# Kernel tuning notes

Hardware: AMD Instinct MI355X
Metric: run time of the kernel (lower is better)

The kernel has to match this reference:

```python
import jax, jax.numpy as jnp
import numpy as np

GRID_SHAPE = (32, 32)
TEMPERATURE = 1.0


def setup_inputs() -> dict:
    key = jax.random.key(0)
    k1, k2 = jax.random.split(key)
    x = jax.random.normal(k1, (16384, 1024), dtype=jnp.float32)
    som_weights = jax.random.normal(k2, (*GRID_SHAPE, 1024), dtype=jnp.float32) * 0.05
    return {"x": x, "som_weights": som_weights}


def reference(x, som_weights):
    # x: [B, D]; som_weights: [G1, G2, D]
    B, D = x.shape
    g1, g2 = GRID_SHAPE
    w_flat = som_weights.reshape(g1 * g2, D)  # [N, D]
    x_sq = jnp.sum(x * x, axis=-1, keepdims=True)          # [B, 1]
    w_sq = jnp.sum(w_flat * w_flat, axis=-1)[None, :]       # [1, N]
    d2 = x_sq - 2.0 * (x @ w_flat.T) + w_sq                 # [B, N]
    logits = (-d2 / TEMPERATURE).reshape(B, g1, g2)         # [B, G1, G2]
    # per-dimension softmax along each spatial axis, combined multiplicatively
    s1 = jax.nn.softmax(logits, axis=1)
    s2 = jax.nn.softmax(logits, axis=2)
    combined = s1 * s2
    combined = combined / (jnp.sum(combined, axis=(1, 2), keepdims=True) + 1e-8)
    # soft reconstruction: weighted sum over grid of codebook vectors
    recon = jnp.einsum('bn,nd->bd', combined.reshape(B, g1 * g2), w_flat)
    return recon
```

## Files before the change

kernel.cpp:

```cpp
#include <hip/hip_runtime.h>
#include <hip/hip_bf16.h>

static constexpr int BATCH = 16384;
static constexpr int DIM   = 1024;
static constexpr int NN    = 1024;
static constexpr int G     = 32;

typedef _Float16 half8  __attribute__((ext_vector_type(8)));
typedef _Float16 half4v __attribute__((ext_vector_type(4)));
typedef float    f32x4  __attribute__((ext_vector_type(4)));

__global__ __launch_bounds__(256) void transpose_w_kernel(const float* __restrict__ W,
                                                          _Float16* __restrict__ Wh,
                                                          _Float16* __restrict__ WTh) {
    __shared__ _Float16 tile[64][72];
    const int t  = threadIdx.x;
    const int n0 = (blockIdx.x & 15) * 64;
    const int d0 = (blockIdx.x >> 4) * 64;
#pragma unroll
    for (int p = 0; p < 4; ++p) {
        int n = n0 + p * 16 + (t >> 4);
        int d = d0 + (t & 15) * 4;
        float4 v = *(const float4*)(W + (size_t)n * DIM + d);
        half4v h;
        h[0] = (_Float16)v.x; h[1] = (_Float16)v.y;
        h[2] = (_Float16)v.z; h[3] = (_Float16)v.w;
        *(half4v*)(Wh + (size_t)n * DIM + d) = h;
#pragma unroll
        for (int k = 0; k < 4; ++k)
            tile[(t & 15) * 4 + k][p * 16 + (t >> 4)] = h[k];
    }
    __syncthreads();
#pragma unroll
    for (int p = 0; p < 4; ++p) {
        int dp = p * 16 + (t >> 4);
        int nc = (t & 15) * 4;
        half4v hv = *(const half4v*)&tile[dp][nc];
        *(half4v*)(WTh + (size_t)(d0 + dp) * NN + n0 + nc) = hv;
    }
}

__global__ __launch_bounds__(256) void wsq_kernel(const float* __restrict__ W,
                                                  float* __restrict__ wsq) {
    const int n = blockIdx.x;
    const int t = threadIdx.x;
    float4 v = *(const float4*)(W + (size_t)n * DIM + 4 * t);
    float ss = v.x * v.x + v.y * v.y + v.z * v.z + v.w * v.w;
#pragma unroll
    for (int o = 32; o > 0; o >>= 1) ss += __shfl_xor(ss, o, 64);
    __shared__ float red[4];
    if ((t & 63) == 0) red[t >> 6] = ss;
    __syncthreads();
    if (t == 0) wsq[n] = red[0] + red[1] + red[2] + red[3];
}

template <typename AT, int EPI>
__global__ __launch_bounds__(256) void gemm_bt_kernel(const AT* __restrict__ A,
                                                      const _Float16* __restrict__ B,
                                                      float* __restrict__ C,
                                                      const float* __restrict__ wsq,
                                                      int M, int N, int K) {
    constexpr bool AF32 = sizeof(AT) == 4;
    __shared__ __align__(16) AT       As[128 * 64];
    __shared__ __align__(16) _Float16 Bs[128 * 64];

    const int t  = threadIdx.x;
    const int l  = t & 63;
    const int wv = t >> 6;

    const int NT  = N >> 7;
    const int MT  = M >> 7;
    const int lid = blockIdx.x;
    const int xcd = lid & 7;
    const int i0  = lid >> 3;
    const int bn  = (i0 % NT) * 128;
    const int bm  = (xcd * (MT >> 3) + i0 / NT) * 128;

    const int wm = (wv >> 1) * 64;
    const int wn = (wv & 1) * 64;

    auto stage = [&](int k0) {
        if constexpr (AF32) {
#pragma unroll
            for (int j = 0; j < 8; ++j) {
                int rbase = wv * 32 + j * 4;
                int row   = rbase + (l >> 4);
                int c     = (l & 15) ^ (row & 15);
                const float* gA = (const float*)A + (size_t)(bm + row) * K + k0 + c * 4;
                __builtin_amdgcn_global_load_lds(
                    (const __attribute__((address_space(1))) void*)gA,
                    (__attribute__((address_space(3))) void*)((float*)As + rbase * 64),
                    16, 0, 0);
            }
        } else {
#pragma unroll
            for (int j = 0; j < 4; ++j) {
                int rbase = wv * 32 + j * 8;
                int row   = rbase + (l >> 3);
                int c     = (l & 7) ^ (row & 7);
                const _Float16* gA = (const _Float16*)A + (size_t)(bm + row) * K + k0 + c * 8;
                __builtin_amdgcn_global_load_lds(
                    (const __attribute__((address_space(1))) void*)gA,
                    (__attribute__((address_space(3))) void*)((_Float16*)As + rbase * 64),
                    16, 0, 0);
            }
        }
#pragma unroll
        for (int j = 0; j < 4; ++j) {
            int rbase = wv * 32 + j * 8;
            int row   = rbase + (l >> 3);
            int c     = (l & 7) ^ (row & 7);
            const _Float16* gB = B + (size_t)(bn + row) * K + k0 + c * 8;
            __builtin_amdgcn_global_load_lds(
                (const __attribute__((address_space(1))) void*)gB,
                (__attribute__((address_space(3))) void*)(Bs + rbase * 64),
                16, 0, 0);
        }
    };

    f32x4 acc[4][4] = {};
    stage(0);

    for (int kt = 0; kt < K; kt += 64) {
        __syncthreads();
#pragma unroll
        for (int sub = 0; sub < 2; ++sub) {
            half8 af[4], bf[4];
#pragma unroll
            for (int mi = 0; mi < 4; ++mi) {
                if constexpr (AF32) {
                    const float* pa = (const float*)As + (wm + (l & 15) + mi * 16) * 64;
                    int cpair = sub * 8 + (l >> 4) * 2;
                    f32x4 lo = *(const f32x4*)(pa + ((cpair     ) ^ (l & 15)) * 4);
                    f32x4 hi = *(const f32x4*)(pa + ((cpair + 1) ^ (l & 15)) * 4);
#pragma unroll
                    for (int q = 0; q < 4; ++q) {
                        af[mi][q]     = (_Float16)lo[q];
                        af[mi][4 + q] = (_Float16)hi[q];
                    }
                } else {
                    const _Float16* pa = (const _Float16*)As + (wm + (l & 15) + mi * 16) * 64;
                    int c = sub * 4 + (l >> 4);
                    af[mi] = *(const half8*)(pa + (c ^ (l & 7)) * 8);
                }
            }
#pragma unroll
            for (int ni = 0; ni < 4; ++ni) {
                const _Float16* pb = Bs + (wn + (l & 15) + ni * 16) * 64;
                int c = sub * 4 + (l >> 4);
                bf[ni] = *(const half8*)(pb + (c ^ (l & 7)) * 8);
            }
#pragma unroll
            for (int mi = 0; mi < 4; ++mi)
#pragma unroll
                for (int ni = 0; ni < 4; ++ni)
                    acc[mi][ni] = __builtin_amdgcn_mfma_f32_16x16x32_f16(
                        af[mi], bf[ni], acc[mi][ni], 0, 0, 0);
        }
        __syncthreads();
        if (kt + 64 < K) stage(kt + 64);
    }

#pragma unroll
    for (int mi = 0; mi < 4; ++mi) {
        const int rbase = bm + wm + mi * 16 + (l >> 4) * 4;
#pragma unroll
        for (int ni = 0; ni < 4; ++ni) {
            const int col = bn + wn + ni * 16 + (l & 15);
            float wq = (EPI == 1) ? wsq[col] : 0.f;
#pragma unroll
            for (int r = 0; r < 4; ++r) {
                float v = acc[mi][ni][r];
                if (EPI == 1) v = 2.f * v - wq;
                C[(size_t)(rbase + r) * N + col] = v;
            }
        }
    }
}

__global__ __launch_bounds__(256) void softmax_kernel(const float* __restrict__ L,
                                                      _Float16* __restrict__ Ch) {
    const int l  = threadIdx.x & 63;
    const int wv = threadIdx.x >> 6;
    const int b  = blockIdx.x * 4 + wv;

    const f32x4* Lr = (const f32x4*)(L + (size_t)b * NN);
    f32x4 v[4];
#pragma unroll
    for (int i = 0; i < 4; ++i) v[i] = Lr[i * 64 + l];

    float er[4][4], ec[4][4];
    float rinv[4];
#pragma unroll
    for (int i = 0; i < 4; ++i) {
        float m = fmaxf(fmaxf(v[i][0], v[i][1]), fmaxf(v[i][2], v[i][3]));
        m = fmaxf(m, __shfl_xor(m, 1, 64));
        m = fmaxf(m, __shfl_xor(m, 2, 64));
        m = fmaxf(m, __shfl_xor(m, 4, 64));
        float s = 0.f;
#pragma unroll
        for (int j = 0; j < 4; ++j) { er[i][j] = __expf(v[i][j] - m); s += er[i][j]; }
        s += __shfl_xor(s, 1, 64);
        s += __shfl_xor(s, 2, 64);
        s += __shfl_xor(s, 4, 64);
        rinv[i] = 1.f / s;
    }
#pragma unroll
    for (int j = 0; j < 4; ++j) {
        float m = fmaxf(fmaxf(v[0][j], v[1][j]), fmaxf(v[2][j], v[3][j]));
        m = fmaxf(m, __shfl_xor(m, 8, 64));
        m = fmaxf(m, __shfl_xor(m, 16, 64));
        m = fmaxf(m, __shfl_xor(m, 32, 64));
        float s = 0.f;
#pragma unroll
        for (int i = 0; i < 4; ++i) { ec[i][j] = __expf(v[i][j] - m); s += ec[i][j]; }
        s += __shfl_xor(s, 8, 64);
        s += __shfl_xor(s, 16, 64);
        s += __shfl_xor(s, 32, 64);
        float ci = 1.f / s;
#pragma unroll
        for (int i = 0; i < 4; ++i) ec[i][j] *= ci;
    }
    float c[4][4];
    float tot = 0.f;
#pragma unroll
    for (int i = 0; i < 4; ++i)
#pragma unroll
        for (int j = 0; j < 4; ++j) {
            c[i][j] = er[i][j] * rinv[i] * ec[i][j];
            tot += c[i][j];
        }
#pragma unroll
    for (int o = 32; o > 0; o >>= 1) tot += __shfl_xor(tot, o, 64);
    float inv = 1.f / (tot + 1e-8f);
#pragma unroll
    for (int i = 0; i < 4; ++i) {
        half4v h;
#pragma unroll
        for (int j = 0; j < 4; ++j) h[j] = (_Float16)(c[i][j] * inv);
        ((half4v*)(Ch + (size_t)b * NN))[i * 64 + l] = h;
    }
}

extern "C" void kernel_launch(void* const* d_in, const int* in_sizes, int n_in,
                              void* d_out, int out_size, void* d_ws, size_t ws_size,
                              hipStream_t stream) {
    const float* x = (const float*)d_in[0];
    const float* w = (const float*)d_in[1];
    float* out = (float*)d_out;

    char* ws = (char*)d_ws;
    size_t off = 0;
    _Float16* ch  = (_Float16*)(ws + off); off += (size_t)BATCH * NN * 2;
    float*    L   = (float*)   (ws + off); off += (size_t)BATCH * NN * 4;
    _Float16* wh  = (_Float16*)(ws + off); off += (size_t)NN * DIM * 2;
    _Float16* wth = (_Float16*)(ws + off); off += (size_t)DIM * NN * 2;
    float*    wsq = (float*)   (ws + off); off += (size_t)NN * 4;

    transpose_w_kernel<<<256, 256, 0, stream>>>(w, wh, wth);
    wsq_kernel<<<NN, 256, 0, stream>>>(w, wsq);
    gemm_bt_kernel<float, 1><<<(BATCH / 128) * (NN / 128), 256, 0, stream>>>(
        x, wh, L, wsq, BATCH, NN, DIM);
    softmax_kernel<<<BATCH / 4, 256, 0, stream>>>(L, ch);
    gemm_bt_kernel<_Float16, 0><<<(BATCH / 128) * (DIM / 128), 256, 0, stream>>>(
        ch, wth, out, nullptr, BATCH, DIM, NN);
}
```

Before: 247.8 us.

## Fuse distance GEMM with 2D softmax, fold wsq into transpose, retile second GEMM

Replaces the first GEMM plus separate softmax kernel with one fused kernel. Each block computes full 32x1024 logit rows in registers, then does the per-axis softmaxes in log space and the normalization, writing fp16 weights directly. This removes the 64MB fp32 logits round trip and one launch. The ||w||^2 reduction moves into the transpose kernel via atomics after a memset, and the second GEMM uses a K-tile of 32 with a new swizzle. The fused kernel reads W fragments straight from global memory without LDS staging and holds 128 accumulators per thread. That risks register pressure and poorer B reuse, and the log-space recombination changes numerics slightly.

```diff
diff --git a/kernel.cpp b/kernel.cpp
--- a/kernel.cpp
+++ b/kernel.cpp
@@ -12,7 +12,8 @@
 
 __global__ __launch_bounds__(256) void transpose_w_kernel(const float* __restrict__ W,
                                                           _Float16* __restrict__ Wh,
-                                                          _Float16* __restrict__ WTh) {
+                                                          _Float16* __restrict__ WTh,
+                                                          float* __restrict__ wsq) {
     __shared__ _Float16 tile[64][72];
     const int t  = threadIdx.x;
     const int n0 = (blockIdx.x & 15) * 64;
@@ -29,6 +30,12 @@
 #pragma unroll
         for (int k = 0; k < 4; ++k)
             tile[(t & 15) * 4 + k][p * 16 + (t >> 4)] = h[k];
+        float ss = v.x * v.x + v.y * v.y + v.z * v.z + v.w * v.w;
+        ss += __shfl_xor(ss, 1, 64);
+        ss += __shfl_xor(ss, 2, 64);
+        ss += __shfl_xor(ss, 4, 64);
+        ss += __shfl_xor(ss, 8, 64);
+        if ((t & 15) == 0) atomicAdd(wsq + n, ss);
     }
     __syncthreads();
 #pragma unroll
@@ -40,29 +47,198 @@
     }
 }
 
-__global__ __launch_bounds__(256) void wsq_kernel(const float* __restrict__ W,
-                                                  float* __restrict__ wsq) {
-    const int n = blockIdx.x;
-    const int t = threadIdx.x;
-    float4 v = *(const float4*)(W + (size_t)n * DIM + 4 * t);
-    float ss = v.x * v.x + v.y * v.y + v.z * v.z + v.w * v.w;
-#pragma unroll
-    for (int o = 32; o > 0; o >>= 1) ss += __shfl_xor(ss, o, 64);
-    __shared__ float red[4];
-    if ((t & 63) == 0) red[t >> 6] = ss;
-    __syncthreads();
-    if (t == 0) wsq[n] = red[0] + red[1] + red[2] + red[3];
+__global__ __launch_bounds__(256, 2) void fused1_kernel(const float* __restrict__ X,
+                                                        const _Float16* __restrict__ Wh,
+                                                        const float* __restrict__ wsq,
+                                                        _Float16* __restrict__ Ch) {
+    __shared__ __align__(16) _Float16 As[2][32 * 64];
+    __shared__ float st[4][32][32];
+    __shared__ float rowtot[4][32];
+
+    const int t  = threadIdx.x;
+    const int l  = t & 63;
+    const int wv = t >> 6;
+    const int b0 = blockIdx.x * 32;
+
+    const int srow = t >> 3;
+    const int schk = t & 7;
+    const int soff = srow * 64 + ((schk ^ (srow & 7)) * 8);
+    const float* xrow = X + (size_t)(b0 + srow) * DIM + schk * 8;
+
+    const int nbase = wv * 256 + (l & 15);
+    const int kfrag = (l >> 4) * 8;
+
+    f32x4 acc[2][16] = {};
+
+    float4 pa = *(const float4*)(xrow);
+    float4 pb = *(const float4*)(xrow + 4);
+
+    auto writeA = [&](int buf, float4 a, float4 b) {
+        half8 h;
+        h[0] = (_Float16)a.x; h[1] = (_Float16)a.y;
+        h[2] = (_Float16)a.z; h[3] = (_Float16)a.w;
+        h[4] = (_Float16)b.x; h[5] = (_Float16)b.y;
+        h[6] = (_Float16)b.z; h[7] = (_Float16)b.w;
+        *(half8*)(&As[buf][soff]) = h;
+    };
+    writeA(0, pa, pb);
+
+    int p = 0;
+    for (int kt = 0; kt < DIM; kt += 64, p ^= 1) {
+        __syncthreads();
+        if (kt + 64 < DIM) {
+            pa = *(const float4*)(xrow + kt + 64);
+            pb = *(const float4*)(xrow + kt + 64 + 4);
+        }
+#pragma unroll
+        for (int sub = 0; sub < 2; ++sub) {
+            const int ck = (sub * 4 + (l >> 4)) ^ (l & 7);
+            half8 af0 = *(const half8*)(&As[p][(l & 15) * 64 + ck * 8]);
+            half8 af1 = *(const half8*)(&As[p][((l & 15) + 16) * 64 + ck * 8]);
+#pragma unroll
+            for (int ni = 0; ni < 16; ++ni) {
+                const _Float16* gb = Wh + (size_t)(nbase + 16 * ni) * DIM + kt + sub * 32 + kfrag;
+                half8 bf = *(const half8*)gb;
+                acc[0][ni] = __builtin_amdgcn_mfma_f32_16x16x32_f16(af0, bf, acc[0][ni], 0, 0, 0);
+                acc[1][ni] = __builtin_amdgcn_mfma_f32_16x16x32_f16(af1, bf, acc[1][ni], 0, 0, 0);
+            }
+        }
+        if (kt + 64 < DIM) writeA(p ^ 1, pa, pb);
+    }
+
+#pragma unroll
+    for (int ni = 0; ni < 16; ++ni) {
+        float wq = wsq[nbase + 16 * ni];
+#pragma unroll
+        for (int mi = 0; mi < 2; ++mi)
+#pragma unroll
+            for (int r = 0; r < 4; ++r)
+                acc[mi][ni][r] = 2.f * acc[mi][ni][r] - wq;
+    }
+
+    float o2[2][8][4];
+#pragma unroll
+    for (int mi = 0; mi < 2; ++mi)
+#pragma unroll
+        for (int n1 = 0; n1 < 8; ++n1)
+#pragma unroll
+            for (int r = 0; r < 4; ++r) {
+                float m = fmaxf(acc[mi][2 * n1][r], acc[mi][2 * n1 + 1][r]);
+                m = fmaxf(m, __shfl_xor(m, 1, 64));
+                m = fmaxf(m, __shfl_xor(m, 2, 64));
+                m = fmaxf(m, __shfl_xor(m, 4, 64));
+                m = fmaxf(m, __shfl_xor(m, 8, 64));
+                float s = __expf(acc[mi][2 * n1][r] - m) + __expf(acc[mi][2 * n1 + 1][r] - m);
+                s += __shfl_xor(s, 1, 64);
+                s += __shfl_xor(s, 2, 64);
+                s += __shfl_xor(s, 4, 64);
+                s += __shfl_xor(s, 8, 64);
+                o2[mi][n1][r] = m + __logf(s);
+            }
+
+    float mfin[2][2][4], o1[2][2][4];
+#pragma unroll
+    for (int mi = 0; mi < 2; ++mi)
+#pragma unroll
+        for (int n0 = 0; n0 < 2; ++n0)
+#pragma unroll
+            for (int r = 0; r < 4; ++r) {
+                float m = -1e30f;
+#pragma unroll
+                for (int n1 = 0; n1 < 8; ++n1)
+                    m = fmaxf(m, acc[mi][2 * n1 + n0][r]);
+                st[wv][mi * 16 + (l >> 4) * 4 + r][n0 * 16 + (l & 15)] = m;
+            }
+    __syncthreads();
+#pragma unroll
+    for (int mi = 0; mi < 2; ++mi)
+#pragma unroll
+        for (int n0 = 0; n0 < 2; ++n0)
+#pragma unroll
+            for (int r = 0; r < 4; ++r) {
+                int b = mi * 16 + (l >> 4) * 4 + r, g2 = n0 * 16 + (l & 15);
+                mfin[mi][n0][r] = fmaxf(fmaxf(st[0][b][g2], st[1][b][g2]),
+                                        fmaxf(st[2][b][g2], st[3][b][g2]));
+            }
+    __syncthreads();
+#pragma unroll
+    for (int mi = 0; mi < 2; ++mi)
+#pragma unroll
+        for (int n0 = 0; n0 < 2; ++n0)
+#pragma unroll
+            for (int r = 0; r < 4; ++r) {
+                float s = 0.f;
+#pragma unroll
+                for (int n1 = 0; n1 < 8; ++n1)
+                    s += __expf(acc[mi][2 * n1 + n0][r] - mfin[mi][n0][r]);
+                st[wv][mi * 16 + (l >> 4) * 4 + r][n0 * 16 + (l & 15)] = s;
+            }
+    __syncthreads();
+#pragma unroll
+    for (int mi = 0; mi < 2; ++mi)
+#pragma unroll
+        for (int n0 = 0; n0 < 2; ++n0)
+#pragma unroll
+            for (int r = 0; r < 4; ++r) {
+                int b = mi * 16 + (l >> 4) * 4 + r, g2 = n0 * 16 + (l & 15);
+                float s = st[0][b][g2] + st[1][b][g2] + st[2][b][g2] + st[3][b][g2];
+                o1[mi][n0][r] = mfin[mi][n0][r] + __logf(s);
+            }
+
+    float tot[2][4] = {};
+#pragma unroll
+    for (int mi = 0; mi < 2; ++mi)
+#pragma unroll
+        for (int ni = 0; ni < 16; ++ni)
+#pragma unroll
+            for (int r = 0; r < 4; ++r) {
+                float c = __expf(2.f * acc[mi][ni][r] - o2[mi][ni >> 1][r] - o1[mi][ni & 1][r]);
+                acc[mi][ni][r] = c;
+                tot[mi][r] += c;
+            }
+#pragma unroll
+    for (int mi = 0; mi < 2; ++mi)
+#pragma unroll
+        for (int r = 0; r < 4; ++r) {
+            float s = tot[mi][r];
+            s += __shfl_xor(s, 1, 64);
+            s += __shfl_xor(s, 2, 64);
+            s += __shfl_xor(s, 4, 64);
+            s += __shfl_xor(s, 8, 64);
+            tot[mi][r] = s;
+        }
+    if ((l & 15) == 0)
+#pragma unroll
+        for (int mi = 0; mi < 2; ++mi)
+#pragma unroll
+            for (int r = 0; r < 4; ++r)
+                rowtot[wv][mi * 16 + (l >> 4) * 4 + r] = tot[mi][r];
+    __syncthreads();
+    float inv[2][4];
+#pragma unroll
+    for (int mi = 0; mi < 2; ++mi)
+#pragma unroll
+        for (int r = 0; r < 4; ++r) {
+            int b = mi * 16 + (l >> 4) * 4 + r;
+            inv[mi][r] = 1.f / (rowtot[0][b] + rowtot[1][b] + rowtot[2][b] + rowtot[3][b] + 1e-8f);
+        }
+#pragma unroll
+    for (int mi = 0; mi < 2; ++mi)
+#pragma unroll
+        for (int r = 0; r < 4; ++r) {
+            size_t row = b0 + mi * 16 + (l >> 4) * 4 + r;
+#pragma unroll
+            for (int ni = 0; ni < 16; ++ni)
+                Ch[row * NN + nbase + 16 * ni] = (_Float16)(acc[mi][ni][r] * inv[mi][r]);
+        }
 }
 
-template <typename AT, int EPI>
-__global__ __launch_bounds__(256) void gemm_bt_kernel(const AT* __restrict__ A,
-                                                      const _Float16* __restrict__ B,
-                                                      float* __restrict__ C,
-                                                      const float* __restrict__ wsq,
-                                                      int M, int N, int K) {
-    constexpr bool AF32 = sizeof(AT) == 4;
-    __shared__ __align__(16) AT       As[128 * 64];
-    __shared__ __align__(16) _Float16 Bs[128 * 64];
+__global__ __launch_bounds__(256) void gemm2_kernel(const _Float16* __restrict__ A,
+                                                    const _Float16* __restrict__ B,
+                                                    float* __restrict__ C,
+                                                    int M, int N, int K) {
+    __shared__ __align__(16) _Float16 As[128 * 32];
+    __shared__ __align__(16) _Float16 Bs[128 * 32];
 
     const int t  = threadIdx.x;
     const int l  = t & 63;
@@ -79,86 +255,48 @@
     const int wm = (wv >> 1) * 64;
     const int wn = (wv & 1) * 64;
 
+    const int srow = (l >> 2);
+    const int skk  = (((l & 3) ^ ((srow >> 1) & 3)) * 8);
+
     auto stage = [&](int k0) {
-        if constexpr (AF32) {
-#pragma unroll
-            for (int j = 0; j < 8; ++j) {
-                int rbase = wv * 32 + j * 4;
-                int row   = rbase + (l >> 4);
-                int c     = (l & 15) ^ (row & 15);
-                const float* gA = (const float*)A + (size_t)(bm + row) * K + k0 + c * 4;
-                __builtin_amdgcn_global_load_lds(
-                    (const __attribute__((address_space(1))) void*)gA,
-                    (__attribute__((address_space(3))) void*)((float*)As + rbase * 64),
-                    16, 0, 0);
-            }
-        } else {
-#pragma unroll
-            for (int j = 0; j < 4; ++j) {
-                int rbase = wv * 32 + j * 8;
-                int row   = rbase + (l >> 3);
-                int c     = (l & 7) ^ (row & 7);
-                const _Float16* gA = (const _Float16*)A + (size_t)(bm + row) * K + k0 + c * 8;
-                __builtin_amdgcn_global_load_lds(
-                    (const __attribute__((address_space(1))) void*)gA,
-                    (__attribute__((address_space(3))) void*)((_Float16*)As + rbase * 64),
-                    16, 0, 0);
-            }
-        }
-#pragma unroll
-        for (int j = 0; j < 4; ++j) {
-            int rbase = wv * 32 + j * 8;
-            int row   = rbase + (l >> 3);
-            int c     = (l & 7) ^ (row & 7);
-            const _Float16* gB = B + (size_t)(bn + row) * K + k0 + c * 8;
+#pragma unroll
+        for (int j = 0; j < 2; ++j) {
+            int rbase = wv * 32 + j * 16;
+            const _Float16* gA = A + (size_t)(bm + rbase + srow) * K + k0 + skk;
+            __builtin_amdgcn_global_load_lds(
+                (const __attribute__((address_space(1))) void*)gA,
+                (__attribute__((address_space(3))) void*)(As + rbase * 32), 16, 0, 0);
+            const _Float16* gB = B + (size_t)(bn + rbase + srow) * K + k0 + skk;
             __builtin_amdgcn_global_load_lds(
                 (const __attribute__((address_space(1))) void*)gB,
-                (__attribute__((address_space(3))) void*)(Bs + rbase * 64),
-                16, 0, 0);
+                (__attribute__((address_space(3))) void*)(Bs + rbase * 32), 16, 0, 0);
         }
     };
 
     f32x4 acc[4][4] = {};
     stage(0);
-
-    for (int kt = 0; kt < K; kt += 64) {
+    const int xr   = ((l & 15) >> 1) & 3;
+    const int kqs  = (((l >> 4) ^ xr) * 8);
+    const int mrow = wm + (l & 15);
+    const int ncol = wn + (l & 15);
+
+    for (int kt = 0; kt < K; kt += 32) {
         __syncthreads();
-#pragma unroll
-        for (int sub = 0; sub < 2; ++sub) {
-            half8 af[4], bf[4];
-#pragma unroll
-            for (int mi = 0; mi < 4; ++mi) {
-                if constexpr (AF32) {
-                    const float* pa = (const float*)As + (wm + (l & 15) + mi * 16) * 64;
-                    int cpair = sub * 8 + (l >> 4) * 2;
-                    f32x4 lo = *(const f32x4*)(pa + ((cpair     ) ^ (l & 15)) * 4);
-                    f32x4 hi = *(const f32x4*)(pa + ((cpair + 1) ^ (l & 15)) * 4);
-#pragma unroll
-                    for (int q = 0; q < 4; ++q) {
-                        af[mi][q]     = (_Float16)lo[q];
-                        af[mi][4 + q] = (_Float16)hi[q];
-                    }
-                } else {
-                    const _Float16* pa = (const _Float16*)As + (wm + (l & 15) + mi * 16) * 64;
-                    int c = sub * 4 + (l >> 4);
-                    af[mi] = *(const half8*)(pa + (c ^ (l & 7)) * 8);
-                }
-            }
-#pragma unroll
-            for (int ni = 0; ni < 4; ++ni) {
-                const _Float16* pb = Bs + (wn + (l & 15) + ni * 16) * 64;
-                int c = sub * 4 + (l >> 4);
-                bf[ni] = *(const half8*)(pb + (c ^ (l & 7)) * 8);
-            }
-#pragma unroll
-            for (int mi = 0; mi < 4; ++mi)
-#pragma unroll
-                for (int ni = 0; ni < 4; ++ni)
-                    acc[mi][ni] = __builtin_amdgcn_mfma_f32_16x16x32_f16(
-                        af[mi], bf[ni], acc[mi][ni], 0, 0, 0);
-        }
+        half8 af[4], bf[4];
+#pragma unroll
+        for (int mi = 0; mi < 4; ++mi)
+            af[mi] = *(const half8*)(As + (mrow + mi * 16) * 32 + kqs);
+#pragma unroll
+        for (int ni = 0; ni < 4; ++ni)
+            bf[ni] = *(const half8*)(Bs + (ncol + ni * 16) * 32 + kqs);
+#pragma unroll
+        for (int mi = 0; mi < 4; ++mi)
+#pragma unroll
+            for (int ni = 0; ni < 4; ++ni)
+                acc[mi][ni] = __builtin_amdgcn_mfma_f32_16x16x32_f16(
+                    af[mi], bf[ni], acc[mi][ni], 0, 0, 0);
         __syncthreads();
-        if (kt + 64 < K) stage(kt + 64);
+        if (kt + 32 < K) stage(kt + 32);
     }
 
 #pragma unroll
@@ -167,78 +305,10 @@
 #pragma unroll
         for (int ni = 0; ni < 4; ++ni) {
             const int col = bn + wn + ni * 16 + (l & 15);
-            float wq = (EPI == 1) ? wsq[col] : 0.f;
-#pragma unroll
-            for (int r = 0; r < 4; ++r) {
-                float v = acc[mi][ni][r];
-                if (EPI == 1) v = 2.f * v - wq;
-                C[(size_t)(rbase + r) * N + col] = v;
-            }
-        }
-    }
-}
-
-__global__ __launch_bounds__(256) void softmax_kernel(const float* __restrict__ L,
-                                                      _Float16* __restrict__ Ch) {
-    const int l  = threadIdx.x & 63;
-    const int wv = threadIdx.x >> 6;
-    const int b  = blockIdx.x * 4 + wv;
-
-    const f32x4* Lr = (const f32x4*)(L + (size_t)b * NN);
-    f32x4 v[4];
-#pragma unroll
-    for (int i = 0; i < 4; ++i) v[i] = Lr[i * 64 + l];
-
-    float er[4][4], ec[4][4];
-    float rinv[4];
-#pragma unroll
-    for (int i = 0; i < 4; ++i) {
-        float m = fmaxf(fmaxf(v[i][0], v[i][1]), fmaxf(v[i][2], v[i][3]));
-        m = fmaxf(m, __shfl_xor(m, 1, 64));
-        m = fmaxf(m, __shfl_xor(m, 2, 64));
-        m = fmaxf(m, __shfl_xor(m, 4, 64));
-        float s = 0.f;
-#pragma unroll
-        for (int j = 0; j < 4; ++j) { er[i][j] = __expf(v[i][j] - m); s += er[i][j]; }
-        s += __shfl_xor(s, 1, 64);
-        s += __shfl_xor(s, 2, 64);
-        s += __shfl_xor(s, 4, 64);
-        rinv[i] = 1.f / s;
-    }
-#pragma unroll
-    for (int j = 0; j < 4; ++j) {
-        float m = fmaxf(fmaxf(v[0][j], v[1][j]), fmaxf(v[2][j], v[3][j]));
-        m = fmaxf(m, __shfl_xor(m, 8, 64));
-        m = fmaxf(m, __shfl_xor(m, 16, 64));
-        m = fmaxf(m, __shfl_xor(m, 32, 64));
-        float s = 0.f;
-#pragma unroll
-        for (int i = 0; i < 4; ++i) { ec[i][j] = __expf(v[i][j] - m); s += ec[i][j]; }
-        s += __shfl_xor(s, 8, 64);
-        s += __shfl_xor(s, 16, 64);
-        s += __shfl_xor(s, 32, 64);
-        float ci = 1.f / s;
-#pragma unroll
-        for (int i = 0; i < 4; ++i) ec[i][j] *= ci;
-    }
-    float c[4][4];
-    float tot = 0.f;
-#pragma unroll
-    for (int i = 0; i < 4; ++i)
-#pragma unroll
-        for (int j = 0; j < 4; ++j) {
-            c[i][j] = er[i][j] * rinv[i] * ec[i][j];
-            tot += c[i][j];
-        }
-#pragma unroll
-    for (int o = 32; o > 0; o >>= 1) tot += __shfl_xor(tot, o, 64);
-    float inv = 1.f / (tot + 1e-8f);
-#pragma unroll
-    for (int i = 0; i < 4; ++i) {
-        half4v h;
-#pragma unroll
-        for (int j = 0; j < 4; ++j) h[j] = (_Float16)(c[i][j] * inv);
-        ((half4v*)(Ch + (size_t)b * NN))[i * 64 + l] = h;
+#pragma unroll
+            for (int r = 0; r < 4; ++r)
+                C[(size_t)(rbase + r) * N + col] = acc[mi][ni][r];
+        }
     }
 }
 
@@ -252,16 +322,13 @@
     char* ws = (char*)d_ws;
     size_t off = 0;
     _Float16* ch  = (_Float16*)(ws + off); off += (size_t)BATCH * NN * 2;
-    float*    L   = (float*)   (ws + off); off += (size_t)BATCH * NN * 4;
     _Float16* wh  = (_Float16*)(ws + off); off += (size_t)NN * DIM * 2;
     _Float16* wth = (_Float16*)(ws + off); off += (size_t)DIM * NN * 2;
     float*    wsq = (float*)   (ws + off); off += (size_t)NN * 4;
 
-    transpose_w_kernel<<<256, 256, 0, stream>>>(w, wh, wth);
-    wsq_kernel<<<NN, 256, 0, stream>>>(w, wsq);
-    gemm_bt_kernel<float, 1><<<(BATCH / 128) * (NN / 128), 256, 0, stream>>>(
-        x, wh, L, wsq, BATCH, NN, DIM);
-    softmax_kernel<<<BATCH / 4, 256, 0, stream>>>(L, ch);
-    gemm_bt_kernel<_Float16, 0><<<(BATCH / 128) * (DIM / 128), 256, 0, stream>>>(
-        ch, wth, out, nullptr, BATCH, DIM, NN);
+    hipMemsetAsync(wsq, 0, NN * sizeof(float), stream);
+    transpose_w_kernel<<<256, 256, 0, stream>>>(w, wh, wth, wsq);
+    fused1_kernel<<<BATCH / 32, 256, 0, stream>>>(x, wh, wsq, ch);
+    gemm2_kernel<<<(BATCH / 128) * (DIM / 128), 256, 0, stream>>>(
+        ch, wth, out, BATCH, DIM, NN);
 }
```

Measured after the change: 314.0 us. 26.7% more time.
